# Kernel optimization log

Hardware: AMD Instinct MI355X
Metric: run time of the kernel (lower is better)

The kernel has to match this reference:

```python
import jax, jax.numpy as jnp
import numpy as np

B = 100000   # batch of nodes
K = 32       # sampled neighbors per node (num_sample)
N = 500000   # total nodes in graph (embedding table rows)
D = 128      # feature dim


def setup_inputs() -> dict:
    key = jax.random.key(0)
    k1, k2 = jax.random.split(key)
    embed_table = jax.random.normal(k1, (N, D), dtype=jnp.float32)
    neigh_idx = jax.random.randint(k2, (B, K), 0, N, dtype=jnp.int64)
    return {"embed_table": embed_table, "neigh_idx": neigh_idx, "num_sample": K}


def reference(embed_table, neigh_idx, num_sample):
    # Original builds a row-normalized dense one-hot mask [B, U] and does
    # mask.mm(embed_matrix): per-row mean of neighbor embeddings.
    # With fixed num_sample, this is exactly a gather + mean over K.
    neigh_feats = embed_table[neigh_idx]          # [B, K, D]
    to_feats = jnp.mean(neigh_feats, axis=1)       # [B, D]
    return to_feats
```

## Files before the change

kernel.cpp:

```cpp
#include <hip/hip_runtime.h>


constexpr int K = 32;
constexpr int D = 128;
constexpr int VEC = D / 4;
constexpr int NODES_PER_BLOCK = 8;
constexpr int BLOCK = NODES_PER_BLOCK * VEC;

__global__ __launch_bounds__(BLOCK)
void mean_agg_kernel(const float4* __restrict__ embed,
                     const int* __restrict__ idx,
                     float4* __restrict__ out,
                     int B) {
    __shared__ int s_idx[NODES_PER_BLOCK * K];

    const int tid  = threadIdx.x;
    const int node = tid >> 5;
    const int vec  = tid & 31;
    const int b0   = blockIdx.x * NODES_PER_BLOCK;

    const long long gidx = (long long)b0 * K + tid;
    if (gidx < (long long)B * K) {
        s_idx[tid] = idx[gidx];
    }
    __syncthreads();

    const int b = b0 + node;
    if (b >= B) return;

    float4 sum = make_float4(0.f, 0.f, 0.f, 0.f);
#pragma unroll
    for (int k = 0; k < K; ++k) {
        const size_t row = (size_t)s_idx[node * K + k];
        const float4 v = embed[row * VEC + vec];
        sum.x += v.x;
        sum.y += v.y;
        sum.z += v.z;
        sum.w += v.w;
    }

    const float inv = 1.0f / (float)K;
    float4 r;
    r.x = sum.x * inv;
    r.y = sum.y * inv;
    r.z = sum.z * inv;
    r.w = sum.w * inv;
    out[(size_t)b * VEC + vec] = r;
}

extern "C" void kernel_launch(void* const* d_in, const int* in_sizes, int n_in,
                              void* d_out, int out_size, void* d_ws, size_t ws_size,
                              hipStream_t stream) {
    const float* embed = (const float*)d_in[0];
    const int*   idx   = (const int*)d_in[1];
    float* out = (float*)d_out;

    const int B = in_sizes[1] / K;

    dim3 grid((B + NODES_PER_BLOCK - 1) / NODES_PER_BLOCK);
    mean_agg_kernel<<<grid, BLOCK, 0, stream>>>(
        (const float4*)embed, idx, (float4*)out, B);
}
```

Baseline: 521.3 us.

## Map one wavefront per node with scalar index loads and batched float2 gathers

Reassigns work so each 64-lane wavefront handles one node, with each lane loading a float2 slice of a 512-byte row. Indices are read as wave-uniform values through readfirstlane, which lets the compiler use scalar loads and removes the shared-memory staging and the block barrier. Gathers are issued in batches of eight independent loads into four accumulators, so more loads are in flight per wave. The trade-off is narrower per-lane loads and fewer nodes per block, and an occupancy hint is added to the launch bounds.

After: 517.9 us. No clear change (-0.6%).

```diff
diff --git a/kernel.cpp b/kernel.cpp
--- a/kernel.cpp
+++ b/kernel.cpp
@@ -3,49 +3,53 @@
 
 constexpr int K = 32;
 constexpr int D = 128;
-constexpr int VEC = D / 4;
-constexpr int NODES_PER_BLOCK = 8;
-constexpr int BLOCK = NODES_PER_BLOCK * VEC;
+constexpr int WAVES_PER_BLOCK = 4;
+constexpr int BLOCK = WAVES_PER_BLOCK * 64;
 
-__global__ __launch_bounds__(BLOCK)
-void mean_agg_kernel(const float4* __restrict__ embed,
+__global__ __launch_bounds__(BLOCK, 8)
+void mean_agg_kernel(const float* __restrict__ embed,
                      const int* __restrict__ idx,
-                     float4* __restrict__ out,
+                     float* __restrict__ out,
                      int B) {
-    __shared__ int s_idx[NODES_PER_BLOCK * K];
+    const int tid  = threadIdx.x;
+    const int lane = tid & 63;
 
-    const int tid  = threadIdx.x;
-    const int node = tid >> 5;
-    const int vec  = tid & 31;
-    const int b0   = blockIdx.x * NODES_PER_BLOCK;
-
-    const long long gidx = (long long)b0 * K + tid;
-    if (gidx < (long long)B * K) {
-        s_idx[tid] = idx[gidx];
-    }
-    __syncthreads();
-
-    const int b = b0 + node;
+    int b = blockIdx.x * WAVES_PER_BLOCK + (tid >> 6);
+    b = __builtin_amdgcn_readfirstlane(b);
     if (b >= B) return;
 
-    float4 sum = make_float4(0.f, 0.f, 0.f, 0.f);
+    const int* __restrict__ idx_b = idx + (size_t)b * K;
+    int rows[K];
 #pragma unroll
     for (int k = 0; k < K; ++k) {
-        const size_t row = (size_t)s_idx[node * K + k];
-        const float4 v = embed[row * VEC + vec];
-        sum.x += v.x;
-        sum.y += v.y;
-        sum.z += v.z;
-        sum.w += v.w;
+        rows[k] = idx_b[k];
+    }
+
+    float2 acc[4];
+    acc[0] = acc[1] = acc[2] = acc[3] = make_float2(0.f, 0.f);
+
+#pragma unroll
+    for (int kk = 0; kk < K; kk += 8) {
+        float2 v[8];
+#pragma unroll
+        for (int j = 0; j < 8; ++j) {
+            const float2* __restrict__ rp =
+                (const float2*)(embed + (size_t)(unsigned)rows[kk + j] * D);
+            v[j] = rp[lane];
+        }
+#pragma unroll
+        for (int j = 0; j < 8; ++j) {
+            acc[j & 3].x += v[j].x;
+            acc[j & 3].y += v[j].y;
+        }
     }
 
     const float inv = 1.0f / (float)K;
-    float4 r;
-    r.x = sum.x * inv;
-    r.y = sum.y * inv;
-    r.z = sum.z * inv;
-    r.w = sum.w * inv;
-    out[(size_t)b * VEC + vec] = r;
+    float2 r;
+    r.x = (acc[0].x + acc[1].x + acc[2].x + acc[3].x) * inv;
+    r.y = (acc[0].y + acc[1].y + acc[2].y + acc[3].y) * inv;
+
+    ((float2*)(out + (size_t)b * D))[lane] = r;
 }
 
 extern "C" void kernel_launch(void* const* d_in, const int* in_sizes, int n_in,
@@ -57,7 +61,6 @@
 
     const int B = in_sizes[1] / K;
 
-    dim3 grid((B + NODES_PER_BLOCK - 1) / NODES_PER_BLOCK);
-    mean_agg_kernel<<<grid, BLOCK, 0, stream>>>(
-        (const float4*)embed, idx, (float4*)out, B);
+    dim3 grid((B + WAVES_PER_BLOCK - 1) / WAVES_PER_BLOCK);
+    mean_agg_kernel<<<grid, BLOCK, 0, stream>>>(embed, idx, out, B);
 }
```
